# Optimization experiments

Hardware: AMD Instinct MI355X
Metric: run time of the kernel (lower is better)

## Reference

```python
import jax, jax.numpy as jnp
import numpy as np

M1 = 32
M2 = 32
S1 = 64
S2 = 64
TWO_PI = jnp.float32(2.0 * np.pi)


def setup_inputs() -> dict:
    key = jax.random.key(0)
    k1, k2, k3, k4, k5 = jax.random.split(key, 5)
    B, C, N = 8, 64, 16384
    x = jax.random.normal(k1, (B, C, N), dtype=jnp.float32)
    x_in = jax.random.uniform(k2, (B, N, 2), dtype=jnp.float32)
    x_out = jax.random.uniform(k3, (B, N, 2), dtype=jnp.float32)
    # xavier_normal for fan_in=64, fan_out=64 over [i,o,m,2]
    std = jnp.float32(np.sqrt(2.0 / (64 + 64)))
    w1 = std * jax.random.normal(k4, (64, 64, M2, 2), dtype=jnp.float32)
    w2 = std * jax.random.normal(k5, (64, 64, M1, 2), dtype=jnp.float32)
    return {"x": x, "x_in": x_in, "x_out": x_out, "w1": w1, "w2": w2}


def reference(x, x_in, x_out, w1, w2):
    # iphi = identity: mapped coords are the mesh coords themselves.
    # Original code repeats the 1-D NUFFT bases along the grid dims (s1/s2)
    # before the einsums; since the repeated axis is constant, the final
    # contraction over it is exactly a factor s1 (resp. s2). We compute the
    # mathematically identical form without materializing [B,N,m,s] tensors.
    Wy = w1[..., 0] + 1j * w1[..., 1]  # [i, o, m2] complex
    Wx = w2[..., 0] + 1j * w2[..., 1]  # [i, o, m1] complex
    ky = jnp.arange(M2, dtype=jnp.float32)
    kx = jnp.arange(M1, dtype=jnp.float32)

    # forward NUFFT bases from x_in  (exp(-i 2 pi k . p))
    bfy = jnp.exp(-1j * TWO_PI * x_in[..., 0:1] * ky)   # [B, N, m2]
    bfx = jnp.exp(-1j * TWO_PI * x_in[..., 1:2] * kx)   # [B, N, m1]
    # inverse NUFFT bases from x_out (exp(+i 2 pi k . p))
    ibfy = jnp.exp(1j * TWO_PI * x_out[..., 0:1] * ky)  # [B, N, m2]
    ibfx = jnp.exp(1j * TWO_PI * x_out[..., 1:2] * kx)  # [B, N, m1]

    xc = x.astype(jnp.complex64)

    # y-direction branch (fourier_weight[0])
    fty = jnp.einsum('bcn,bny->bcy', xc, bfy)           # [B, in, m2]
    my = jnp.einsum('biy,ioy->boy', fty, Wy)            # [B, out, m2]
    xy = S1 * jnp.einsum('boy,bny->bon', my, ibfy).real  # [B, out, N]

    # x-direction branch (fourier_weight[1])
    ftx = jnp.einsum('bcn,bnx->bcx', xc, bfx)           # [B, in, m1]
    mx = jnp.einsum('bix,iox->box', ftx, Wx)            # [B, out, m1]
    xx = S2 * jnp.einsum('box,bnx->bon', mx, ibfx).real  # [B, out, N]

    return xx + xy
```

## Files before the change

### kernel.cpp

```cpp
#include <hip/hip_runtime.h>

#define BB 8
#define CC 64
#define OO 64
#define NN 16384
#define MMODE 32
#define JJ 128
#define SFAC 64.0f

typedef __attribute__((ext_vector_type(8))) short short8;
typedef __attribute__((ext_vector_type(4))) float f32x4;

static __device__ __forceinline__ unsigned short f2bf(float f) {
  unsigned u = __float_as_uint(f);
  u += 0x7FFF + ((u >> 16) & 1);
  return (unsigned short)(u >> 16);
}
static __device__ __forceinline__ unsigned pack2(float a, float b) {
  return (unsigned)f2bf(a) | ((unsigned)f2bf(b) << 16);
}
static __device__ __forceinline__ float sin2pi(float x) { return __builtin_amdgcn_sinf(x); }
static __device__ __forceinline__ float cos2pi(float x) { return __builtin_amdgcn_cosf(x); }


__global__ __launch_bounds__(256) void fwd_kernel(
    const float* __restrict__ x, const float* __restrict__ x_in,
    float* __restrict__ ft) {
  __shared__ __attribute__((aligned(16))) short bas[JJ * 72];
  __shared__ __attribute__((aligned(16))) short xs[64 * 72];
  __shared__ __attribute__((aligned(16))) float ps[512];
  const int t = threadIdx.x;
  const int b = blockIdx.y, sl = blockIdx.x;
  const int n0 = sl * 256;

  if (t < 128) {
    const float4 v = *(const float4*)&x_in[((size_t)b * NN + n0) * 2 + t * 4];
    *(float4*)&ps[t * 4] = v;
  }
  const int xc = t >> 2, xq = t & 3;
  const float* xbase = x + ((size_t)(b * CC + xc)) * NN + n0;
  float4 cur[4];
#pragma unroll
  for (int k = 0; k < 4; ++k) cur[k] = *(const float4*)&xbase[(k * 4 + xq) * 4];

  const int w = t >> 6, L = t & 63;
  const int q4 = L >> 4, l15 = L & 15;
  f32x4 acc[8];
#pragma unroll
  for (int i = 0; i < 8; ++i) acc[i] = (f32x4){0.f, 0.f, 0.f, 0.f};

  __syncthreads();

  for (int s = 0; s < 4; ++s) {
#pragma unroll
    for (int k = 0; k < 4; ++k)
      *(uint2*)&xs[xc * 72 + (k * 4 + xq) * 4] =
          make_uint2(pack2(cur[k].x, cur[k].y), pack2(cur[k].z, cur[k].w));
    if (s < 3) {
#pragma unroll
      for (int k = 0; k < 4; ++k)
        cur[k] = *(const float4*)&xbase[(s + 1) * 64 + (k * 4 + xq) * 4];
    }
#pragma unroll
    for (int ti = 0; ti < 2; ++ti) {
      const int tau = t + ti * 256;
      const int ng = tau & 7, mm = tau >> 3;
      const int br = mm >> 5, m = mm & 31;
      const float fm = (float)m;
      union { unsigned short u[8]; uint4 v; } R, I;
#pragma unroll
      for (int k = 0; k < 8; ++k) {
        const float p = ps[(s * 64 + ng * 8 + k) * 2 + br];
        float rev = fm * p;
        rev -= floorf(rev);
        R.u[k] = f2bf(cos2pi(rev));
        I.u[k] = f2bf(-sin2pi(rev));
      }
      const int row = br * 64 + 2 * m;
      *(uint4*)&bas[row * 72 + ng * 8]       = R.v;
      *(uint4*)&bas[(row + 1) * 72 + ng * 8] = I.v;
    }
    __syncthreads();
#pragma unroll
    for (int ks = 0; ks < 2; ++ks) {
      const int ko = ks * 32 + q4 * 8;
      const short8 a0 = *(const short8*)&bas[(w * 32 + l15) * 72 + ko];
      const short8 a1 = *(const short8*)&bas[(w * 32 + 16 + l15) * 72 + ko];
#pragma unroll
      for (int ct = 0; ct < 4; ++ct) {
        const short8 bv = *(const short8*)&xs[(ct * 16 + l15) * 72 + ko];
        acc[ct]     = __builtin_amdgcn_mfma_f32_16x16x32_bf16(a0, bv, acc[ct], 0, 0, 0);
        acc[4 + ct] = __builtin_amdgcn_mfma_f32_16x16x32_bf16(a1, bv, acc[4 + ct], 0, 0, 0);
      }
    }
    __syncthreads();
  }
#pragma unroll
  for (int ai = 0; ai < 2; ++ai)
#pragma unroll
    for (int ct = 0; ct < 4; ++ct) {
      const f32x4 v = acc[ai * 4 + ct];
#pragma unroll
      for (int r = 0; r < 4; ++r)
        atomicAdd(&ft[((size_t)b * JJ + w * 32 + ai * 16 + q4 * 4 + r) * CC + ct * 16 + l15], v[r]);
    }
}

__global__ __launch_bounds__(256) void mix_kernel(
    const float* __restrict__ ft, const float* __restrict__ w1,
    const float* __restrict__ w2, float* __restrict__ A) {
  __shared__ float red[8][64];
  __shared__ float fre[64], fim[64];
  const int m = blockIdx.x, branch = blockIdx.y, b = blockIdx.z;
  const int t = threadIdx.x;
  const int c = t & 63, g = t >> 6;
  const int jb = branch * 64 + 2 * m;
  if (t < 64) fre[t] = ft[((size_t)b * JJ + jb) * CC + t];
  else if (t < 128) fim[t - 64] = ft[((size_t)b * JJ + jb + 1) * CC + (t - 64)];
  __syncthreads();
  const float* w = branch ? w2 : w1;
  float ar = 0.f, ai = 0.f;
#pragma unroll 4
  for (int ii = 0; ii < 16; ++ii) {
    const int i = g * 16 + ii;
    const float2 wv = *(const float2*)&w[(((size_t)i * 64 + c) * MMODE + m) * 2];
    ar += fre[i] * wv.x - fim[i] * wv.y;
    ai += fre[i] * wv.y + fim[i] * wv.x;
  }
  red[g * 2][c] = ar;
  red[g * 2 + 1][c] = ai;
  __syncthreads();
  if (t < 64) {
    const float sr = red[0][t] + red[2][t] + red[4][t] + red[6][t];
    const float si = red[1][t] + red[3][t] + red[5][t] + red[7][t];
    *(float2*)&A[((size_t)b * OO + t) * JJ + jb] = make_float2(SFAC * sr, -SFAC * si);
  }
}

__global__ __launch_bounds__(256) void inv_kernel(
    const float* __restrict__ x_out, const float* __restrict__ A,
    float* __restrict__ out) {
  __shared__ __attribute__((aligned(16))) short As_s[OO * 136];
  __shared__ __attribute__((aligned(16))) short basn[64 * 136];
  __shared__ __attribute__((aligned(16))) float psI[512];
  const int t = threadIdx.x;
  const int b = blockIdx.y;
  const int n0 = blockIdx.x * 256;

  if (t < 128) {
    const float4 v = *(const float4*)&x_out[((size_t)b * NN + n0) * 2 + t * 4];
    *(float4*)&psI[t * 4] = v;
  }
#pragma unroll
  for (int idx = t; idx < 2048; idx += 256) {
    const int o = idx >> 5, j4 = idx & 31;
    const float4 v = *(const float4*)&A[((size_t)b * OO + o) * JJ + j4 * 4];
    *(uint2*)&As_s[o * 136 + j4 * 4] = make_uint2(pack2(v.x, v.y), pack2(v.z, v.w));
  }
  const int w = t >> 6, L = t & 63;
  const int q4 = L >> 4, l15 = L & 15;
  const int nl = t & 63, q = t >> 6, br = q >> 1, half = q & 1;
  const int ot0 = (w & 1) * 32;
  const int nt0 = (w >> 1) * 32;
  __syncthreads();

  for (int s = 0; s < 4; ++s) {
    {
      const float p = psI[(s * 64 + nl) * 2 + br];
      const float fr = p - floorf(p);
      const float s1 = sin2pi(fr), c1 = cos2pi(fr);
      float brr = 1.f, bii = 0.f;
      if (half) {
        float r = c1, qq = s1;
#pragma unroll
        for (int k = 0; k < 4; ++k) { const float nr = r*r - qq*qq, ni = 2.f*r*qq; r = nr; qq = ni; }
        brr = r; bii = qq;
      }
      short* bp = &basn[nl * 136 + br * 64 + half * 32];
#pragma unroll
      for (int g = 0; g < 4; ++g) {
        union { unsigned short u[8]; uint4 v; } P;
#pragma unroll
        for (int mi = 0; mi < 4; ++mi) {
          P.u[2 * mi]     = f2bf(brr);
          P.u[2 * mi + 1] = f2bf(bii);
          const float nr = brr * c1 - bii * s1, ni = brr * s1 + bii * c1;
          brr = nr; bii = ni;
        }
        *(uint4*)&bp[g * 8] = P.v;
      }
    }
    __syncthreads();
    f32x4 acc[4];
#pragma unroll
    for (int i = 0; i < 4; ++i) acc[i] = (f32x4){0.f, 0.f, 0.f, 0.f};
#pragma unroll
    for (int ks = 0; ks < 4; ++ks) {
      const int ko = ks * 32 + q4 * 8;
      const short8 a0 = *(const short8*)&As_s[(ot0 + l15) * 136 + ko];
      const short8 a1 = *(const short8*)&As_s[(ot0 + 16 + l15) * 136 + ko];
      const short8 b0 = *(const short8*)&basn[(nt0 + l15) * 136 + ko];
      const short8 b1 = *(const short8*)&basn[(nt0 + 16 + l15) * 136 + ko];
      acc[0] = __builtin_amdgcn_mfma_f32_16x16x32_bf16(a0, b0, acc[0], 0, 0, 0);
      acc[1] = __builtin_amdgcn_mfma_f32_16x16x32_bf16(a0, b1, acc[1], 0, 0, 0);
      acc[2] = __builtin_amdgcn_mfma_f32_16x16x32_bf16(a1, b0, acc[2], 0, 0, 0);
      acc[3] = __builtin_amdgcn_mfma_f32_16x16x32_bf16(a1, b1, acc[3], 0, 0, 0);
    }
    const int nbase = n0 + s * 64 + nt0 + l15;
#pragma unroll
    for (int oi = 0; oi < 2; ++oi)
#pragma unroll
      for (int ni = 0; ni < 2; ++ni) {
        const f32x4 v = acc[oi * 2 + ni];
#pragma unroll
        for (int r = 0; r < 4; ++r)
          out[((size_t)b * OO + ot0 + oi * 16 + q4 * 4 + r) * NN + nbase + ni * 16] = v[r];
      }
    __syncthreads();
  }
}

extern "C" void kernel_launch(void* const* d_in, const int* in_sizes, int n_in,
                              void* d_out, int out_size, void* d_ws, size_t ws_size,
                              hipStream_t stream) {
  const float* x     = (const float*)d_in[0];
  const float* x_in  = (const float*)d_in[1];
  const float* x_out = (const float*)d_in[2];
  const float* w1    = (const float*)d_in[3];
  const float* w2    = (const float*)d_in[4];
  float* out = (float*)d_out;
  float* ft = (float*)d_ws;
  float* A  = ft + (size_t)BB * JJ * CC;

  hipMemsetAsync(ft, 0, (size_t)BB * JJ * CC * sizeof(float), stream);
  fwd_kernel<<<dim3(64, BB), 256, 0, stream>>>(x, x_in, ft);
  mix_kernel<<<dim3(MMODE, 2, BB), 256, 0, stream>>>(ft, w1, w2, A);
  inv_kernel<<<dim3(64, BB), 256, 0, stream>>>(x_out, A, out);
}
```

Measured before the change: 125.5 us.

## Fuse forward, mix and inverse into one persistent kernel with grid barriers

Merges the three kernels into a single 512-block launch separated by two atomic-counter grid barriers, and removes the large memset of the accumulator. The forward stage now writes per-slice partial results to workspace instead of using atomics, and the mix stage reduces those partials itself. This is meant to cut launch gaps and atomic contention. In exchange it adds spin-wait barriers that depend on all 512 blocks being resident at once, plus a larger partial-sum buffer to read back.

```diff
diff --git a/kernel.cpp b/kernel.cpp
--- a/kernel.cpp
+++ b/kernel.cpp
@@ -7,6 +7,7 @@
 #define MMODE 32
 #define JJ 128
 #define SFAC 64.0f
+#define NBLK 512u
 
 typedef __attribute__((ext_vector_type(8))) short short8;
 typedef __attribute__((ext_vector_type(4))) float f32x4;
@@ -22,201 +23,232 @@
 static __device__ __forceinline__ float sin2pi(float x) { return __builtin_amdgcn_sinf(x); }
 static __device__ __forceinline__ float cos2pi(float x) { return __builtin_amdgcn_cosf(x); }
 
-
-__global__ __launch_bounds__(256) void fwd_kernel(
+static __device__ __forceinline__ void gbar(unsigned* ctr, unsigned target) {
+  __syncthreads();
+  if (threadIdx.x == 0) {
+    __threadfence();
+    __hip_atomic_fetch_add(ctr, 1u, __ATOMIC_ACQ_REL, __HIP_MEMORY_SCOPE_AGENT);
+    while (__hip_atomic_load(ctr, __ATOMIC_ACQUIRE, __HIP_MEMORY_SCOPE_AGENT) < target) {}
+    __threadfence();
+  }
+  __syncthreads();
+}
+
+
+__global__ __launch_bounds__(256, 2) void fused_kernel(
     const float* __restrict__ x, const float* __restrict__ x_in,
-    float* __restrict__ ft) {
-  __shared__ __attribute__((aligned(16))) short bas[JJ * 72];
-  __shared__ __attribute__((aligned(16))) short xs[64 * 72];
-  __shared__ __attribute__((aligned(16))) float ps[512];
+    const float* __restrict__ x_out, const float* __restrict__ w1,
+    const float* __restrict__ w2, float* __restrict__ out,
+    float* __restrict__ part, float* __restrict__ A, unsigned* __restrict__ ctr) {
+  __shared__ __attribute__((aligned(16))) unsigned char smem[37376];
   const int t = threadIdx.x;
-  const int b = blockIdx.y, sl = blockIdx.x;
-  const int n0 = sl * 256;
-
-  if (t < 128) {
-    const float4 v = *(const float4*)&x_in[((size_t)b * NN + n0) * 2 + t * 4];
-    *(float4*)&ps[t * 4] = v;
-  }
-  const int xc = t >> 2, xq = t & 3;
-  const float* xbase = x + ((size_t)(b * CC + xc)) * NN + n0;
-  float4 cur[4];
-#pragma unroll
-  for (int k = 0; k < 4; ++k) cur[k] = *(const float4*)&xbase[(k * 4 + xq) * 4];
-
-  const int w = t >> 6, L = t & 63;
-  const int q4 = L >> 4, l15 = L & 15;
-  f32x4 acc[8];
-#pragma unroll
-  for (int i = 0; i < 8; ++i) acc[i] = (f32x4){0.f, 0.f, 0.f, 0.f};
-
-  __syncthreads();
-
-  for (int s = 0; s < 4; ++s) {
-#pragma unroll
-    for (int k = 0; k < 4; ++k)
-      *(uint2*)&xs[xc * 72 + (k * 4 + xq) * 4] =
-          make_uint2(pack2(cur[k].x, cur[k].y), pack2(cur[k].z, cur[k].w));
-    if (s < 3) {
+  const int blk = blockIdx.x;
+  const int b = blk >> 6, sl = blk & 63;
+
+  {
+    short* bas = (short*)smem;
+    short* xs  = bas + JJ * 72;
+    float* ps  = (float*)(xs + 64 * 72);
+    const int n0 = sl * 256;
+
+    if (t < 128) {
+      const float4 v = *(const float4*)&x_in[((size_t)b * NN + n0) * 2 + t * 4];
+      *(float4*)&ps[t * 4] = v;
+    }
+    const int xc = t >> 2, xq = t & 3;
+    const float* xbase = x + ((size_t)(b * CC + xc)) * NN + n0;
+    float4 cur[4];
+#pragma unroll
+    for (int k = 0; k < 4; ++k) cur[k] = *(const float4*)&xbase[(k * 4 + xq) * 4];
+
+    const int w = t >> 6, L = t & 63;
+    const int q4 = L >> 4, l15 = L & 15;
+    f32x4 acc[8];
+#pragma unroll
+    for (int i = 0; i < 8; ++i) acc[i] = (f32x4){0.f, 0.f, 0.f, 0.f};
+
+    __syncthreads();
+
+    for (int s = 0; s < 4; ++s) {
 #pragma unroll
       for (int k = 0; k < 4; ++k)
-        cur[k] = *(const float4*)&xbase[(s + 1) * 64 + (k * 4 + xq) * 4];
-    }
-#pragma unroll
-    for (int ti = 0; ti < 2; ++ti) {
-      const int tau = t + ti * 256;
-      const int ng = tau & 7, mm = tau >> 3;
-      const int br = mm >> 5, m = mm & 31;
-      const float fm = (float)m;
-      union { unsigned short u[8]; uint4 v; } R, I;
-#pragma unroll
-      for (int k = 0; k < 8; ++k) {
-        const float p = ps[(s * 64 + ng * 8 + k) * 2 + br];
-        float rev = fm * p;
-        rev -= floorf(rev);
-        R.u[k] = f2bf(cos2pi(rev));
-        I.u[k] = f2bf(-sin2pi(rev));
-      }
-      const int row = br * 64 + 2 * m;
-      *(uint4*)&bas[row * 72 + ng * 8]       = R.v;
-      *(uint4*)&bas[(row + 1) * 72 + ng * 8] = I.v;
-    }
-    __syncthreads();
-#pragma unroll
-    for (int ks = 0; ks < 2; ++ks) {
-      const int ko = ks * 32 + q4 * 8;
-      const short8 a0 = *(const short8*)&bas[(w * 32 + l15) * 72 + ko];
-      const short8 a1 = *(const short8*)&bas[(w * 32 + 16 + l15) * 72 + ko];
+        *(uint2*)&xs[xc * 72 + (k * 4 + xq) * 4] =
+            make_uint2(pack2(cur[k].x, cur[k].y), pack2(cur[k].z, cur[k].w));
+      if (s < 3) {
+#pragma unroll
+        for (int k = 0; k < 4; ++k)
+          cur[k] = *(const float4*)&xbase[(s + 1) * 64 + (k * 4 + xq) * 4];
+      }
+#pragma unroll
+      for (int ti = 0; ti < 2; ++ti) {
+        const int tau = t + ti * 256;
+        const int ng = tau & 7, mm = tau >> 3;
+        const int br = mm >> 5, m = mm & 31;
+        const float fm = (float)m;
+        union { unsigned short u[8]; uint4 v; } R, I;
+#pragma unroll
+        for (int k = 0; k < 8; ++k) {
+          const float p = ps[(s * 64 + ng * 8 + k) * 2 + br];
+          float rev = fm * p;
+          rev -= floorf(rev);
+          R.u[k] = f2bf(cos2pi(rev));
+          I.u[k] = f2bf(-sin2pi(rev));
+        }
+        const int row = br * 64 + 2 * m;
+        *(uint4*)&bas[row * 72 + ng * 8]       = R.v;
+        *(uint4*)&bas[(row + 1) * 72 + ng * 8] = I.v;
+      }
+      __syncthreads();
+#pragma unroll
+      for (int ks = 0; ks < 2; ++ks) {
+        const int ko = ks * 32 + q4 * 8;
+        const short8 a0 = *(const short8*)&bas[(w * 32 + l15) * 72 + ko];
+        const short8 a1 = *(const short8*)&bas[(w * 32 + 16 + l15) * 72 + ko];
+#pragma unroll
+        for (int ct = 0; ct < 4; ++ct) {
+          const short8 bv = *(const short8*)&xs[(ct * 16 + l15) * 72 + ko];
+          acc[ct]     = __builtin_amdgcn_mfma_f32_16x16x32_bf16(a0, bv, acc[ct], 0, 0, 0);
+          acc[4 + ct] = __builtin_amdgcn_mfma_f32_16x16x32_bf16(a1, bv, acc[4 + ct], 0, 0, 0);
+        }
+      }
+      __syncthreads();
+    }
+    float* pp = part + (size_t)(b * 64 + sl) * JJ * CC;
+#pragma unroll
+    for (int ai = 0; ai < 2; ++ai)
 #pragma unroll
       for (int ct = 0; ct < 4; ++ct) {
-        const short8 bv = *(const short8*)&xs[(ct * 16 + l15) * 72 + ko];
-        acc[ct]     = __builtin_amdgcn_mfma_f32_16x16x32_bf16(a0, bv, acc[ct], 0, 0, 0);
-        acc[4 + ct] = __builtin_amdgcn_mfma_f32_16x16x32_bf16(a1, bv, acc[4 + ct], 0, 0, 0);
-      }
-    }
-    __syncthreads();
-  }
-#pragma unroll
-  for (int ai = 0; ai < 2; ++ai)
-#pragma unroll
-    for (int ct = 0; ct < 4; ++ct) {
-      const f32x4 v = acc[ai * 4 + ct];
-#pragma unroll
-      for (int r = 0; r < 4; ++r)
-        atomicAdd(&ft[((size_t)b * JJ + w * 32 + ai * 16 + q4 * 4 + r) * CC + ct * 16 + l15], v[r]);
-    }
-}
-
-__global__ __launch_bounds__(256) void mix_kernel(
-    const float* __restrict__ ft, const float* __restrict__ w1,
-    const float* __restrict__ w2, float* __restrict__ A) {
-  __shared__ float red[8][64];
-  __shared__ float fre[64], fim[64];
-  const int m = blockIdx.x, branch = blockIdx.y, b = blockIdx.z;
-  const int t = threadIdx.x;
-  const int c = t & 63, g = t >> 6;
-  const int jb = branch * 64 + 2 * m;
-  if (t < 64) fre[t] = ft[((size_t)b * JJ + jb) * CC + t];
-  else if (t < 128) fim[t - 64] = ft[((size_t)b * JJ + jb + 1) * CC + (t - 64)];
-  __syncthreads();
-  const float* w = branch ? w2 : w1;
-  float ar = 0.f, ai = 0.f;
+        const f32x4 v = acc[ai * 4 + ct];
+#pragma unroll
+        for (int r = 0; r < 4; ++r)
+          pp[(w * 32 + ai * 16 + q4 * 4 + r) * CC + ct * 16 + l15] = v[r];
+      }
+  }
+
+  gbar(ctr, NBLK);
+
+  {
+    float* red = (float*)smem;
+    float* fre = red + 512;
+    float* fim = fre + 64;
+    const int m = blk & 31, branch = (blk >> 5) & 1, b2 = blk >> 6;
+    const int c = t & 63, g = t >> 6;
+    const int jb = branch * 64 + 2 * m;
+    float pre = 0.f, pim = 0.f;
+#pragma unroll
+    for (int k = 0; k < 16; ++k) {
+      const int sl2 = g + 4 * k;
+      const float* pp = part + (size_t)(b2 * 64 + sl2) * JJ * CC;
+      pre += pp[jb * CC + c];
+      pim += pp[(jb + 1) * CC + c];
+    }
+    red[(g * 2) * 64 + c] = pre;
+    red[(g * 2 + 1) * 64 + c] = pim;
+    __syncthreads();
+    if (t < 64) {
+      fre[t] = red[0 * 64 + t] + red[2 * 64 + t] + red[4 * 64 + t] + red[6 * 64 + t];
+      fim[t] = red[1 * 64 + t] + red[3 * 64 + t] + red[5 * 64 + t] + red[7 * 64 + t];
+    }
+    __syncthreads();
+    const float* w = branch ? w2 : w1;
+    float ar = 0.f, ai = 0.f;
 #pragma unroll 4
-  for (int ii = 0; ii < 16; ++ii) {
-    const int i = g * 16 + ii;
-    const float2 wv = *(const float2*)&w[(((size_t)i * 64 + c) * MMODE + m) * 2];
-    ar += fre[i] * wv.x - fim[i] * wv.y;
-    ai += fre[i] * wv.y + fim[i] * wv.x;
-  }
-  red[g * 2][c] = ar;
-  red[g * 2 + 1][c] = ai;
-  __syncthreads();
-  if (t < 64) {
-    const float sr = red[0][t] + red[2][t] + red[4][t] + red[6][t];
-    const float si = red[1][t] + red[3][t] + red[5][t] + red[7][t];
-    *(float2*)&A[((size_t)b * OO + t) * JJ + jb] = make_float2(SFAC * sr, -SFAC * si);
-  }
-}
-
-__global__ __launch_bounds__(256) void inv_kernel(
-    const float* __restrict__ x_out, const float* __restrict__ A,
-    float* __restrict__ out) {
-  __shared__ __attribute__((aligned(16))) short As_s[OO * 136];
-  __shared__ __attribute__((aligned(16))) short basn[64 * 136];
-  __shared__ __attribute__((aligned(16))) float psI[512];
-  const int t = threadIdx.x;
-  const int b = blockIdx.y;
-  const int n0 = blockIdx.x * 256;
-
-  if (t < 128) {
-    const float4 v = *(const float4*)&x_out[((size_t)b * NN + n0) * 2 + t * 4];
-    *(float4*)&psI[t * 4] = v;
-  }
-#pragma unroll
-  for (int idx = t; idx < 2048; idx += 256) {
-    const int o = idx >> 5, j4 = idx & 31;
-    const float4 v = *(const float4*)&A[((size_t)b * OO + o) * JJ + j4 * 4];
-    *(uint2*)&As_s[o * 136 + j4 * 4] = make_uint2(pack2(v.x, v.y), pack2(v.z, v.w));
-  }
-  const int w = t >> 6, L = t & 63;
-  const int q4 = L >> 4, l15 = L & 15;
-  const int nl = t & 63, q = t >> 6, br = q >> 1, half = q & 1;
-  const int ot0 = (w & 1) * 32;
-  const int nt0 = (w >> 1) * 32;
-  __syncthreads();
-
-  for (int s = 0; s < 4; ++s) {
-    {
-      const float p = psI[(s * 64 + nl) * 2 + br];
-      const float fr = p - floorf(p);
-      const float s1 = sin2pi(fr), c1 = cos2pi(fr);
-      float brr = 1.f, bii = 0.f;
-      if (half) {
-        float r = c1, qq = s1;
-#pragma unroll
-        for (int k = 0; k < 4; ++k) { const float nr = r*r - qq*qq, ni = 2.f*r*qq; r = nr; qq = ni; }
-        brr = r; bii = qq;
-      }
-      short* bp = &basn[nl * 136 + br * 64 + half * 32];
-#pragma unroll
-      for (int g = 0; g < 4; ++g) {
-        union { unsigned short u[8]; uint4 v; } P;
-#pragma unroll
-        for (int mi = 0; mi < 4; ++mi) {
-          P.u[2 * mi]     = f2bf(brr);
-          P.u[2 * mi + 1] = f2bf(bii);
-          const float nr = brr * c1 - bii * s1, ni = brr * s1 + bii * c1;
-          brr = nr; bii = ni;
-        }
-        *(uint4*)&bp[g * 8] = P.v;
-      }
-    }
-    __syncthreads();
-    f32x4 acc[4];
-#pragma unroll
-    for (int i = 0; i < 4; ++i) acc[i] = (f32x4){0.f, 0.f, 0.f, 0.f};
-#pragma unroll
-    for (int ks = 0; ks < 4; ++ks) {
-      const int ko = ks * 32 + q4 * 8;
-      const short8 a0 = *(const short8*)&As_s[(ot0 + l15) * 136 + ko];
-      const short8 a1 = *(const short8*)&As_s[(ot0 + 16 + l15) * 136 + ko];
-      const short8 b0 = *(const short8*)&basn[(nt0 + l15) * 136 + ko];
-      const short8 b1 = *(const short8*)&basn[(nt0 + 16 + l15) * 136 + ko];
-      acc[0] = __builtin_amdgcn_mfma_f32_16x16x32_bf16(a0, b0, acc[0], 0, 0, 0);
-      acc[1] = __builtin_amdgcn_mfma_f32_16x16x32_bf16(a0, b1, acc[1], 0, 0, 0);
-      acc[2] = __builtin_amdgcn_mfma_f32_16x16x32_bf16(a1, b0, acc[2], 0, 0, 0);
-      acc[3] = __builtin_amdgcn_mfma_f32_16x16x32_bf16(a1, b1, acc[3], 0, 0, 0);
-    }
-    const int nbase = n0 + s * 64 + nt0 + l15;
-#pragma unroll
-    for (int oi = 0; oi < 2; ++oi)
-#pragma unroll
-      for (int ni = 0; ni < 2; ++ni) {
-        const f32x4 v = acc[oi * 2 + ni];
-#pragma unroll
-        for (int r = 0; r < 4; ++r)
-          out[((size_t)b * OO + ot0 + oi * 16 + q4 * 4 + r) * NN + nbase + ni * 16] = v[r];
-      }
-    __syncthreads();
+    for (int ii = 0; ii < 16; ++ii) {
+      const int i = g * 16 + ii;
+      const float2 wv = *(const float2*)&w[(((size_t)i * 64 + c) * MMODE + m) * 2];
+      ar += fre[i] * wv.x - fim[i] * wv.y;
+      ai += fre[i] * wv.y + fim[i] * wv.x;
+    }
+    __syncthreads();
+    red[(g * 2) * 64 + c] = ar;
+    red[(g * 2 + 1) * 64 + c] = ai;
+    __syncthreads();
+    if (t < 64) {
+      const float sr = red[0 * 64 + t] + red[2 * 64 + t] + red[4 * 64 + t] + red[6 * 64 + t];
+      const float si = red[1 * 64 + t] + red[3 * 64 + t] + red[5 * 64 + t] + red[7 * 64 + t];
+      *(float2*)&A[((size_t)b2 * OO + t) * JJ + jb] = make_float2(SFAC * sr, -SFAC * si);
+    }
+  }
+
+  gbar(ctr, 2u * NBLK);
+
+  {
+    short* As_s = (short*)smem;
+    short* basn = As_s + OO * 136;
+    float* psI  = (float*)(basn + 64 * 136);
+    const int n0 = sl * 256;
+
+    if (t < 128) {
+      const float4 v = *(const float4*)&x_out[((size_t)b * NN + n0) * 2 + t * 4];
+      *(float4*)&psI[t * 4] = v;
+    }
+#pragma unroll
+    for (int idx = t; idx < 2048; idx += 256) {
+      const int o = idx >> 5, j4 = idx & 31;
+      const float4 v = *(const float4*)&A[((size_t)b * OO + o) * JJ + j4 * 4];
+      *(uint2*)&As_s[o * 136 + j4 * 4] = make_uint2(pack2(v.x, v.y), pack2(v.z, v.w));
+    }
+    const int w = t >> 6, L = t & 63;
+    const int q4 = L >> 4, l15 = L & 15;
+    const int nl = t & 63, q = t >> 6, br = q >> 1, half = q & 1;
+    const int ot0 = (w & 1) * 32;
+    const int nt0 = (w >> 1) * 32;
+    __syncthreads();
+
+    for (int s = 0; s < 4; ++s) {
+      {
+        const float p = psI[(s * 64 + nl) * 2 + br];
+        const float fr = p - floorf(p);
+        const float s1 = sin2pi(fr), c1 = cos2pi(fr);
+        float brr = 1.f, bii = 0.f;
+        if (half) {
+          float r = c1, qq = s1;
+#pragma unroll
+          for (int k = 0; k < 4; ++k) { const float nr = r*r - qq*qq, ni = 2.f*r*qq; r = nr; qq = ni; }
+          brr = r; bii = qq;
+        }
+        short* bp = &basn[nl * 136 + br * 64 + half * 32];
+#pragma unroll
+        for (int g2 = 0; g2 < 4; ++g2) {
+          union { unsigned short u[8]; uint4 v; } P;
+#pragma unroll
+          for (int mi = 0; mi < 4; ++mi) {
+            P.u[2 * mi]     = f2bf(brr);
+            P.u[2 * mi + 1] = f2bf(bii);
+            const float nr = brr * c1 - bii * s1, ni = brr * s1 + bii * c1;
+            brr = nr; bii = ni;
+          }
+          *(uint4*)&bp[g2 * 8] = P.v;
+        }
+      }
+      __syncthreads();
+      f32x4 acc[4];
+#pragma unroll
+      for (int i = 0; i < 4; ++i) acc[i] = (f32x4){0.f, 0.f, 0.f, 0.f};
+#pragma unroll
+      for (int ks = 0; ks < 4; ++ks) {
+        const int ko = ks * 32 + q4 * 8;
+        const short8 a0 = *(const short8*)&As_s[(ot0 + l15) * 136 + ko];
+        const short8 a1 = *(const short8*)&As_s[(ot0 + 16 + l15) * 136 + ko];
+        const short8 b0 = *(const short8*)&basn[(nt0 + l15) * 136 + ko];
+        const short8 b1 = *(const short8*)&basn[(nt0 + 16 + l15) * 136 + ko];
+        acc[0] = __builtin_amdgcn_mfma_f32_16x16x32_bf16(a0, b0, acc[0], 0, 0, 0);
+        acc[1] = __builtin_amdgcn_mfma_f32_16x16x32_bf16(a0, b1, acc[1], 0, 0, 0);
+        acc[2] = __builtin_amdgcn_mfma_f32_16x16x32_bf16(a1, b0, acc[2], 0, 0, 0);
+        acc[3] = __builtin_amdgcn_mfma_f32_16x16x32_bf16(a1, b1, acc[3], 0, 0, 0);
+      }
+      const int nbase = n0 + s * 64 + nt0 + l15;
+#pragma unroll
+      for (int oi = 0; oi < 2; ++oi)
+#pragma unroll
+        for (int ni = 0; ni < 2; ++ni) {
+          const f32x4 v = acc[oi * 2 + ni];
+#pragma unroll
+          for (int r = 0; r < 4; ++r)
+            out[((size_t)b * OO + ot0 + oi * 16 + q4 * 4 + r) * NN + nbase + ni * 16] = v[r];
+        }
+      __syncthreads();
+    }
   }
 }
 
@@ -229,11 +261,10 @@
   const float* w1    = (const float*)d_in[3];
   const float* w2    = (const float*)d_in[4];
   float* out = (float*)d_out;
-  float* ft = (float*)d_ws;
-  float* A  = ft + (size_t)BB * JJ * CC;
-
-  hipMemsetAsync(ft, 0, (size_t)BB * JJ * CC * sizeof(float), stream);
-  fwd_kernel<<<dim3(64, BB), 256, 0, stream>>>(x, x_in, ft);
-  mix_kernel<<<dim3(MMODE, 2, BB), 256, 0, stream>>>(ft, w1, w2, A);
-  inv_kernel<<<dim3(64, BB), 256, 0, stream>>>(x_out, A, out);
-}
+  float* part = (float*)d_ws;
+  float* A    = part + (size_t)BB * 64 * JJ * CC;
+  unsigned* ctr = (unsigned*)(A + (size_t)BB * OO * JJ);
+
+  hipMemsetAsync(ctr, 0, 64, stream);
+  fused_kernel<<<dim3(NBLK), 256, 0, stream>>>(x, x_in, x_out, w1, w2, out, part, A, ctr);
+}
```

After: 288.8 us. +130.1%, slower.
